# Kernel optimization log

Hardware: AMD Instinct MI355X
Metric: run time of the kernel (lower is better)

## Reference

```python
import jax, jax.numpy as jnp
import numpy as np

N_NODES = 100000
N_EDGES = 1600000
NUM_FEATURES = 256
HIDDEN_DIM = 128
NUM_CLASSES = 16


def setup_inputs() -> dict:
    key = jax.random.key(0)
    k1, k2, k3, k4 = jax.random.split(key, 4)
    x = jax.random.normal(k1, (N_NODES, NUM_FEATURES), dtype=jnp.float32)
    edge_index = jax.random.randint(k2, (2, N_EDGES), 0, N_NODES, dtype=jnp.int64)
    # Glorot-style init like PyG GCNConv's Linear
    W1 = jax.random.normal(k3, (NUM_FEATURES, HIDDEN_DIM), dtype=jnp.float32) / np.sqrt(NUM_FEATURES)
    b1 = jnp.zeros((HIDDEN_DIM,), dtype=jnp.float32)
    W2 = jax.random.normal(k4, (HIDDEN_DIM, NUM_CLASSES), dtype=jnp.float32) / np.sqrt(HIDDEN_DIM)
    b2 = jnp.zeros((NUM_CLASSES,), dtype=jnp.float32)
    return {"x": x, "edge_index": edge_index, "W1": W1, "b1": b1, "W2": W2, "b2": b2}


def _gcn_norm(edge_index, num_nodes):
    """PyG GCNConv default: add self-loops, symmetric deg^{-1/2} A deg^{-1/2} norm."""
    loops = jnp.arange(num_nodes, dtype=edge_index.dtype)
    row = jnp.concatenate([edge_index[0], loops])  # source
    col = jnp.concatenate([edge_index[1], loops])  # target
    deg = jax.ops.segment_sum(jnp.ones_like(col, dtype=jnp.float32), col,
                              num_segments=num_nodes)
    dinv = jnp.where(deg > 0, jax.lax.rsqrt(deg), 0.0)
    norm = dinv[row] * dinv[col]  # [E + N]
    return row, col, norm


def _gcn_conv(h, row, col, norm, num_nodes):
    # transform first (PyG: lin then propagate), then normalized sum-aggregate
    msg = h[row] * norm[:, None]            # [E+N, d] gather + scale
    return jax.ops.segment_sum(msg, col, num_segments=num_nodes)


def reference(x, edge_index, W1, b1, W2, b2):
    num_nodes = x.shape[0]
    row, col, norm = _gcn_norm(edge_index, num_nodes)
    h = x @ W1
    h = _gcn_conv(h, row, col, norm, num_nodes) + b1
    h = jax.nn.relu(h)
    h = h @ W2
    out = _gcn_conv(h, row, col, norm, num_nodes) + b2
    return out
```

## Files before the change

kernel.cpp:

```cpp
#include <hip/hip_runtime.h>

#define N_NODES 100000
#define N_EDGES 1600000
#define F_IN    256
#define F_HID   128
#define F_OUT   16

#define BSHIFT  9
#define BNODES  512
#define NB      196
#define ECAP    16384
#define CHUNK   4096
#define NCHUNK  ((N_EDGES + CHUNK - 1) / CHUNK)

typedef __attribute__((ext_vector_type(8))) short short8;
typedef __attribute__((ext_vector_type(4))) float float4v;

typedef __attribute__((address_space(1))) const void g_void;
typedef __attribute__((address_space(3))) void lds_void;

__device__ __forceinline__ unsigned int bf16_rn(float f) {
    unsigned int u = __float_as_uint(f);
    return (u + 0x7FFFu + ((u >> 16) & 1u)) >> 16;
}
__device__ __forceinline__ unsigned int cvtpk(float lo, float hi) {
    unsigned int r;
    asm("v_cvt_pk_bf16_f32 %0, %1, %2" : "=v"(r) : "v"(lo), "v"(hi));
    return r;
}
__device__ __forceinline__ float blo(unsigned int u) { return __uint_as_float(u << 16); }
__device__ __forceinline__ float bhi(unsigned int u) { return __uint_as_float(u & 0xFFFF0000u); }
__device__ __forceinline__ float bfu(unsigned short u) { return __uint_as_float(((unsigned int)u) << 16); }


__global__ __launch_bounds__(256) void k_binit(int* __restrict__ bcur) {
    int i = threadIdx.x;
    if (i < NB) bcur[i] = i * ECAP;
}

__global__ __launch_bounds__(256) void k_binscatter(const int* __restrict__ rowi,
                                                    const int* __restrict__ coli,
                                                    int* __restrict__ bcur,
                                                    unsigned int* __restrict__ ebuf) {
    __shared__ int cnt[NB], gbase[NB], run[NB];
    int tid = threadIdx.x;
    int e0 = blockIdx.x * CHUNK;
    for (int i = tid; i < NB; i += 256) { cnt[i] = 0; run[i] = 0; }
    __syncthreads();
    int d[16], s[16];
    #pragma unroll
    for (int i = 0; i < 16; i++) {
        int e = e0 + i * 256 + tid;
        if (e < N_EDGES) {
            d[i] = coli[e]; s[i] = rowi[e];
            atomicAdd(&cnt[d[i] >> BSHIFT], 1);
        } else d[i] = -1;
    }
    __syncthreads();
    for (int i = tid; i < NB; i += 256)
        gbase[i] = cnt[i] ? atomicAdd(&bcur[i], cnt[i]) : 0;
    __syncthreads();
    #pragma unroll
    for (int i = 0; i < 16; i++) {
        if (d[i] >= 0) {
            int b = d[i] >> BSHIFT;
            int off = atomicAdd(&run[b], 1);
            ebuf[gbase[b] + off] = ((unsigned int)(d[i] & 511) << 17) | (unsigned int)s[i];
        }
    }
}

__global__ __launch_bounds__(512) void k_finalize(const int* __restrict__ bcur,
                                                  const unsigned int* __restrict__ ebuf,
                                                  int* __restrict__ rp_start,
                                                  int* __restrict__ rp_end,
                                                  float* __restrict__ dinv,
                                                  int* __restrict__ esrc) {
    __shared__ int ndeg[BNODES];
    __shared__ int sc[BNODES];
    int tid = threadIdx.x;
    int b   = blockIdx.x;
    int nb0 = b << BSHIFT;
    int ebeg = b * ECAP, eend = bcur[b];
    ndeg[tid] = 0;
    __syncthreads();
    for (int e = ebeg + tid; e < eend; e += 512)
        atomicAdd(&ndeg[ebuf[e] >> 17], 1);
    __syncthreads();
    sc[tid] = ndeg[tid];
    __syncthreads();
    for (int off = 1; off < BNODES; off <<= 1) {
        int v = (tid >= off) ? sc[tid - off] : 0;
        __syncthreads();
        sc[tid] += v;
        __syncthreads();
    }
    {
        int n = nb0 + tid;
        int deg = ndeg[tid];
        int excl = sc[tid] - deg;
        if (n < N_NODES) {
            rp_start[n] = ebeg + excl;
            rp_end[n]   = ebeg + excl + deg;
            dinv[n]     = rsqrtf(1.0f + (float)deg);
        }
        ndeg[tid] = excl;
    }
    __syncthreads();
    for (int e = ebeg + tid; e < eend; e += 512) {
        unsigned int p = ebuf[e];
        int off = atomicAdd(&ndeg[p >> 17], 1);
        esrc[ebeg + off] = (int)(p & 0x1FFFFu);
    }
}


__global__ __launch_bounds__(256) void k_transW(const float* __restrict__ W1,
                                                ushort* __restrict__ Wt) {
    int t = blockIdx.x * 256 + threadIdx.x;
    int c = t & 127, k = t >> 7;
    Wt[c * 256 + k] = (ushort)cvtpk(W1[k * 128 + c], 0.f);
}


__global__ __launch_bounds__(256) void k_gemm1(const float* __restrict__ x,
                                               const ushort* __restrict__ Wt,
                                               const float* __restrict__ dinv,
                                               ushort* __restrict__ g1) {
    __shared__ float lx[2][128][32];
    const int tid = threadIdx.x;
    const int wv = tid >> 6;
    const int l  = tid & 63;
    const int m  = l & 15;
    const int q  = l >> 4;
    const int R0 = blockIdx.x * 128;

    #pragma unroll
    for (int r = 0; r < 4; r++) {
        int rt = r * 32 + wv * 8 + (l >> 3);
        int c16 = l & 7;
        int grow = R0 + rt; if (grow > N_NODES - 1) grow = N_NODES - 1;
        const float* src = x + (size_t)grow * F_IN + ((c16 ^ (rt & 7)) << 2);
        float* dst = &lx[0][r * 32 + wv * 8][0];
        __builtin_amdgcn_global_load_lds((g_void*)src, (lds_void*)dst, 16, 0, 0);
    }

    short8 wf[2][8];
    #pragma unroll
    for (int ng = 0; ng < 2; ng++)
        #pragma unroll
        for (int kt = 0; kt < 8; kt++)
            wf[ng][kt] = *(const short8*)&Wt[(wv * 32 + ng * 16 + m) * 256 + kt * 32 + q * 8];

    float4v acc[8][2];
    #pragma unroll
    for (int rg = 0; rg < 8; rg++) {
        acc[rg][0] = (float4v){0.f, 0.f, 0.f, 0.f};
        acc[rg][1] = (float4v){0.f, 0.f, 0.f, 0.f};
    }

    __syncthreads();

    #pragma unroll
    for (int kt = 0; kt < 8; kt++) {
        const int buf = kt & 1;
        if (kt < 7) {
            #pragma unroll
            for (int r = 0; r < 4; r++) {
                int rt = r * 32 + wv * 8 + (l >> 3);
                int c16 = l & 7;
                int grow = R0 + rt; if (grow > N_NODES - 1) grow = N_NODES - 1;
                const float* src = x + (size_t)grow * F_IN + (kt + 1) * 32
                                     + ((c16 ^ (rt & 7)) << 2);
                float* dst = &lx[buf ^ 1][r * 32 + wv * 8][0];
                __builtin_amdgcn_global_load_lds((g_void*)src, (lds_void*)dst, 16, 0, 0);
            }
        }
        #pragma unroll
        for (int rg = 0; rg < 8; rg++) {
            int rt = rg * 16 + m, sw = rt & 7;
            float4 e0 = *(const float4*)&lx[buf][rt][((2 * q)     ^ sw) * 4];
            float4 e1 = *(const float4*)&lx[buf][rt][((2 * q + 1) ^ sw) * 4];
            short8 af;
            ((uint*)&af)[0] = cvtpk(e0.x, e0.y); ((uint*)&af)[1] = cvtpk(e0.z, e0.w);
            ((uint*)&af)[2] = cvtpk(e1.x, e1.y); ((uint*)&af)[3] = cvtpk(e1.z, e1.w);
            acc[rg][0] = __builtin_amdgcn_mfma_f32_16x16x32_bf16(af, wf[0][kt], acc[rg][0], 0, 0, 0);
            acc[rg][1] = __builtin_amdgcn_mfma_f32_16x16x32_bf16(af, wf[1][kt], acc[rg][1], 0, 0, 0);
        }
        __syncthreads();
    }

    #pragma unroll
    for (int rg = 0; rg < 8; rg++) {
        #pragma unroll
        for (int r = 0; r < 4; r++) {
            int row = R0 + rg * 16 + q * 4 + r;
            if (row < N_NODES) {
                float dv = dinv[row];
                float f0 = dv * acc[rg][0][r];
                float f1 = dv * acc[rg][1][r];
                g1[row * F_HID + wv * 32 + m]      = (ushort)cvtpk(f0, f0);
                g1[row * F_HID + wv * 32 + 16 + m] = (ushort)cvtpk(f1, f1);
            }
        }
    }
}


__global__ __launch_bounds__(256) void k_agg1g2(const int* __restrict__ rp_start,
                                                const int* __restrict__ rp_end,
                                                const int* __restrict__ esrc,
                                                const float* __restrict__ dinv,
                                                const unsigned int* __restrict__ g1,
                                                const float* __restrict__ b1,
                                                const float* __restrict__ W2,
                                                ushort* __restrict__ g2b,
                                                int nbase) {
    __shared__ float hl[4][132];
    const int tid  = threadIdx.x;
    const int wave = tid >> 6;
    const int lane = tid & 63;
    const int col  = lane & 15, part = lane >> 4;

    float w2r[32];
    #pragma unroll
    for (int i = 0; i < 32; i++) w2r[i] = W2[i * 64 + lane];

    float2 bb = ((const float2*)b1)[lane];

    #pragma unroll 1
    for (int j = 0; j < 4; j++) {
        const int node = nbase + blockIdx.x * 16 + j * 4 + wave;
        int s = rp_start[node], t = rp_end[node];
        unsigned int u = g1[node * 64 + lane];
        float ax = blo(u), ay = bhi(u);
        int e = s;
        for (; e + 7 < t; e += 8) {
            int r0 = esrc[e],     r1 = esrc[e + 1], r2 = esrc[e + 2], r3 = esrc[e + 3];
            int r4 = esrc[e + 4], r5 = esrc[e + 5], r6 = esrc[e + 6], r7 = esrc[e + 7];
            unsigned int u0 = g1[r0 * 64 + lane], u1 = g1[r1 * 64 + lane];
            unsigned int u2 = g1[r2 * 64 + lane], u3 = g1[r3 * 64 + lane];
            unsigned int u4 = g1[r4 * 64 + lane], u5 = g1[r5 * 64 + lane];
            unsigned int u6 = g1[r6 * 64 + lane], u7 = g1[r7 * 64 + lane];
            ax += blo(u0) + blo(u1) + blo(u2) + blo(u3)
                + blo(u4) + blo(u5) + blo(u6) + blo(u7);
            ay += bhi(u0) + bhi(u1) + bhi(u2) + bhi(u3)
                + bhi(u4) + bhi(u5) + bhi(u6) + bhi(u7);
        }
        for (; e + 3 < t; e += 4) {
            int r0 = esrc[e], r1 = esrc[e + 1], r2 = esrc[e + 2], r3 = esrc[e + 3];
            unsigned int u0 = g1[r0 * 64 + lane], u1 = g1[r1 * 64 + lane];
            unsigned int u2 = g1[r2 * 64 + lane], u3 = g1[r3 * 64 + lane];
            ax += blo(u0) + blo(u1) + blo(u2) + blo(u3);
            ay += bhi(u0) + bhi(u1) + bhi(u2) + bhi(u3);
        }
        for (; e < t; e++) {
            unsigned int u0 = g1[esrc[e] * 64 + lane];
            ax += blo(u0); ay += bhi(u0);
        }
        float wv = dinv[node];
        hl[wave][lane * 2]     = fmaxf(fmaf(wv, ax, bb.x), 0.0f);
        hl[wave][lane * 2 + 1] = fmaxf(fmaf(wv, ay, bb.y), 0.0f);

        float acc = 0.f;
        #pragma unroll
        for (int i = 0; i < 32; i++)
            acc = fmaf(hl[wave][i * 4 + part], w2r[i], acc);
        acc += __shfl_xor(acc, 16);
        acc += __shfl_xor(acc, 32);
        if (lane < 16) g2b[node * 16 + col] = (ushort)bf16_rn(wv * acc);
    }
}


__global__ __launch_bounds__(256) void k_agg2(const int* __restrict__ rp_start,
                                              const int* __restrict__ rp_end,
                                              const int* __restrict__ esrc,
                                              const float* __restrict__ dinv,
                                              const ushort* __restrict__ g2b,
                                              const float* __restrict__ b2,
                                              float* __restrict__ out) {
    int gid = blockIdx.x * 256 + threadIdx.x;
    int node = gid >> 4;
    int f = gid & 15;
    if (node >= N_NODES) return;
    int s = rp_start[node], t = rp_end[node];
    float acc = bfu(g2b[node * 16 + f]);
    int e = s;
    for (; e + 7 < t; e += 8) {
        float a0 = bfu(g2b[esrc[e] * 16 + f]),     a1 = bfu(g2b[esrc[e + 1] * 16 + f]);
        float a2 = bfu(g2b[esrc[e + 2] * 16 + f]), a3 = bfu(g2b[esrc[e + 3] * 16 + f]);
        float a4 = bfu(g2b[esrc[e + 4] * 16 + f]), a5 = bfu(g2b[esrc[e + 5] * 16 + f]);
        float a6 = bfu(g2b[esrc[e + 6] * 16 + f]), a7 = bfu(g2b[esrc[e + 7] * 16 + f]);
        acc += a0 + a1 + a2 + a3 + a4 + a5 + a6 + a7;
    }
    for (; e + 3 < t; e += 4) {
        acc += bfu(g2b[esrc[e] * 16 + f]) + bfu(g2b[esrc[e + 1] * 16 + f])
             + bfu(g2b[esrc[e + 2] * 16 + f]) + bfu(g2b[esrc[e + 3] * 16 + f]);
    }
    for (; e < t; e++) acc += bfu(g2b[esrc[e] * 16 + f]);
    out[node * 16 + f] = fmaf(dinv[node], acc, b2[f]);
}


extern "C" void kernel_launch(void* const* d_in, const int* in_sizes, int n_in,
                              void* d_out, int out_size, void* d_ws, size_t ws_size,
                              hipStream_t stream) {
    const float* x   = (const float*)d_in[0];
    const int*   ei  = (const int*)d_in[1];
    const float* W1  = (const float*)d_in[2];
    const float* b1  = (const float*)d_in[3];
    const float* W2  = (const float*)d_in[4];
    const float* b2  = (const float*)d_in[5];
    float* out = (float*)d_out;

    const int* rowi = ei;
    const int* coli = ei + N_EDGES;

    char* ws = (char*)d_ws;
    int*          bcur     = (int*)(ws + 0);
    int*          rp_start = (int*)(ws + 8192);
    int*          rp_end   = (int*)(ws + 524288);
    float*        dinv     = (float*)(ws + 1048576);
    unsigned int* ebuf     = (unsigned int*)(ws + 2097152);
    int*          esrc     = (int*)(ws + 16777216);
    ushort*       Wt       = (ushort*)(ws + 31457280);
    ushort*       g1       = (ushort*)(ws + 33554432);
    ushort*       g2b      = (ushort*)(ws + 62914560);

    k_binit     <<<1, 256, 0, stream>>>(bcur);
    k_binscatter<<<NCHUNK, 256, 0, stream>>>(rowi, coli, bcur, ebuf);
    k_finalize  <<<NB, 512, 0, stream>>>(bcur, ebuf, rp_start, rp_end, dinv, esrc);
    k_transW    <<<128, 256, 0, stream>>>(W1, Wt);

    k_gemm1     <<<(N_NODES + 127) / 128, 256, 0, stream>>>(x, Wt, dinv, g1);
    k_agg1g2    <<<N_NODES / 32, 256, 0, stream>>>(rp_start, rp_end, esrc, dinv,
                                                   (const unsigned int*)g1, b1, W2, g2b, 0);
    k_agg1g2    <<<N_NODES / 32, 256, 0, stream>>>(rp_start, rp_end, esrc, dinv,
                                                   (const unsigned int*)g1, b1, W2, g2b,
                                                   N_NODES / 2);
    k_agg2      <<<(N_NODES * 16 + 255) / 256, 256, 0, stream>>>(rp_start, rp_end, esrc,
                                                                 dinv, g2b, b2, out);
}
```

Baseline: 328.6 us.

## Replace LDS staging in GEMM1 with register double-buffered loads; split aggregation launches

After: 356.3 us. +8.4%, slower.

```diff
diff --git a/kernel.cpp b/kernel.cpp
--- a/kernel.cpp
+++ b/kernel.cpp
@@ -15,9 +15,6 @@
 
 typedef __attribute__((ext_vector_type(8))) short short8;
 typedef __attribute__((ext_vector_type(4))) float float4v;
-
-typedef __attribute__((address_space(1))) const void g_void;
-typedef __attribute__((address_space(3))) void lds_void;
 
 __device__ __forceinline__ unsigned int bf16_rn(float f) {
     unsigned int u = __float_as_uint(f);
@@ -127,7 +124,6 @@
                                                const ushort* __restrict__ Wt,
                                                const float* __restrict__ dinv,
                                                ushort* __restrict__ g1) {
-    __shared__ float lx[2][128][32];
     const int tid = threadIdx.x;
     const int wv = tid >> 6;
     const int l  = tid & 63;
@@ -135,16 +131,6 @@
     const int q  = l >> 4;
     const int R0 = blockIdx.x * 128;
 
-    #pragma unroll
-    for (int r = 0; r < 4; r++) {
-        int rt = r * 32 + wv * 8 + (l >> 3);
-        int c16 = l & 7;
-        int grow = R0 + rt; if (grow > N_NODES - 1) grow = N_NODES - 1;
-        const float* src = x + (size_t)grow * F_IN + ((c16 ^ (rt & 7)) << 2);
-        float* dst = &lx[0][r * 32 + wv * 8][0];
-        __builtin_amdgcn_global_load_lds((g_void*)src, (lds_void*)dst, 16, 0, 0);
-    }
-
     short8 wf[2][8];
     #pragma unroll
     for (int ng = 0; ng < 2; ng++)
@@ -152,58 +138,56 @@
         for (int kt = 0; kt < 8; kt++)
             wf[ng][kt] = *(const short8*)&Wt[(wv * 32 + ng * 16 + m) * 256 + kt * 32 + q * 8];
 
-    float4v acc[8][2];
-    #pragma unroll
-    for (int rg = 0; rg < 8; rg++) {
-        acc[rg][0] = (float4v){0.f, 0.f, 0.f, 0.f};
-        acc[rg][1] = (float4v){0.f, 0.f, 0.f, 0.f};
-    }
-
-    __syncthreads();
-
-    #pragma unroll
-    for (int kt = 0; kt < 8; kt++) {
-        const int buf = kt & 1;
-        if (kt < 7) {
-            #pragma unroll
-            for (int r = 0; r < 4; r++) {
-                int rt = r * 32 + wv * 8 + (l >> 3);
-                int c16 = l & 7;
-                int grow = R0 + rt; if (grow > N_NODES - 1) grow = N_NODES - 1;
-                const float* src = x + (size_t)grow * F_IN + (kt + 1) * 32
-                                     + ((c16 ^ (rt & 7)) << 2);
-                float* dst = &lx[buf ^ 1][r * 32 + wv * 8][0];
-                __builtin_amdgcn_global_load_lds((g_void*)src, (lds_void*)dst, 16, 0, 0);
-            }
-        }
-        #pragma unroll
-        for (int rg = 0; rg < 8; rg++) {
-            int rt = rg * 16 + m, sw = rt & 7;
-            float4 e0 = *(const float4*)&lx[buf][rt][((2 * q)     ^ sw) * 4];
-            float4 e1 = *(const float4*)&lx[buf][rt][((2 * q + 1) ^ sw) * 4];
-            short8 af;
-            ((uint*)&af)[0] = cvtpk(e0.x, e0.y); ((uint*)&af)[1] = cvtpk(e0.z, e0.w);
-            ((uint*)&af)[2] = cvtpk(e1.x, e1.y); ((uint*)&af)[3] = cvtpk(e1.z, e1.w);
-            acc[rg][0] = __builtin_amdgcn_mfma_f32_16x16x32_bf16(af, wf[0][kt], acc[rg][0], 0, 0, 0);
-            acc[rg][1] = __builtin_amdgcn_mfma_f32_16x16x32_bf16(af, wf[1][kt], acc[rg][1], 0, 0, 0);
-        }
-        __syncthreads();
-    }
-
-    #pragma unroll
-    for (int rg = 0; rg < 8; rg++) {
-        #pragma unroll
-        for (int r = 0; r < 4; r++) {
-            int row = R0 + rg * 16 + q * 4 + r;
-            if (row < N_NODES) {
-                float dv = dinv[row];
-                float f0 = dv * acc[rg][0][r];
-                float f1 = dv * acc[rg][1][r];
-                g1[row * F_HID + wv * 32 + m]      = (ushort)cvtpk(f0, f0);
-                g1[row * F_HID + wv * 32 + 16 + m] = (ushort)cvtpk(f1, f1);
-            }
-        }
-    }
+#define ROWPTR(rg) ({ int grow_ = R0 + (rg) * 16 + m;                          \
+                      if (grow_ > N_NODES - 1) grow_ = N_NODES - 1;            \
+                      x + (size_t)grow_ * F_IN + q * 8; })
+
+#define LOADRG(buf, rg) { const float* p_ = ROWPTR(rg);                        \
+    _Pragma("unroll")                                                          \
+    for (int kt_ = 0; kt_ < 8; kt_++) {                                        \
+        buf[2 * kt_]     = *(const float4*)&p_[kt_ * 32];                      \
+        buf[2 * kt_ + 1] = *(const float4*)&p_[kt_ * 32 + 4];                  \
+    } }
+
+#define CONSUME(buf, rg) {                                                     \
+    float4v a0_ = (float4v){0.f, 0.f, 0.f, 0.f};                               \
+    float4v a1_ = (float4v){0.f, 0.f, 0.f, 0.f};                               \
+    _Pragma("unroll")                                                          \
+    for (int kt_ = 0; kt_ < 8; kt_++) {                                        \
+        short8 af_;                                                            \
+        ((uint*)&af_)[0] = cvtpk(buf[2 * kt_].x,     buf[2 * kt_].y);          \
+        ((uint*)&af_)[1] = cvtpk(buf[2 * kt_].z,     buf[2 * kt_].w);          \
+        ((uint*)&af_)[2] = cvtpk(buf[2 * kt_ + 1].x, buf[2 * kt_ + 1].y);      \
+        ((uint*)&af_)[3] = cvtpk(buf[2 * kt_ + 1].z, buf[2 * kt_ + 1].w);      \
+        a0_ = __builtin_amdgcn_mfma_f32_16x16x32_bf16(af_, wf[0][kt_], a0_, 0, 0, 0); \
+        a1_ = __builtin_amdgcn_mfma_f32_16x16x32_bf16(af_, wf[1][kt_], a1_, 0, 0, 0); \
+    }                                                                          \
+    _Pragma("unroll")                                                          \
+    for (int r_ = 0; r_ < 4; r_++) {                                           \
+        int row_ = R0 + (rg) * 16 + q * 4 + r_;                                \
+        if (row_ < N_NODES) {                                                  \
+            float dv_ = dinv[row_];                                            \
+            float f0_ = dv_ * a0_[r_];                                         \
+            float f1_ = dv_ * a1_[r_];                                         \
+            g1[row_ * F_HID + wv * 32 + m]      = (ushort)cvtpk(f0_, f0_);     \
+            g1[row_ * F_HID + wv * 32 + 16 + m] = (ushort)cvtpk(f1_, f1_);     \
+        }                                                                      \
+    } }
+
+    float4 xa[16], xb[16];
+    LOADRG(xa, 0);
+    LOADRG(xb, 1);
+    CONSUME(xa, 0);  LOADRG(xa, 2);
+    CONSUME(xb, 1);  LOADRG(xb, 3);
+    CONSUME(xa, 2);  LOADRG(xa, 4);
+    CONSUME(xb, 3);  LOADRG(xb, 5);
+    CONSUME(xa, 4);  LOADRG(xa, 6);
+    CONSUME(xb, 5);  LOADRG(xb, 7);
+    CONSUME(xa, 6);
+    CONSUME(xb, 7);
+#undef ROWPTR
+#undef LOADRG
+#undef CONSUME
 }
 
 
@@ -215,7 +199,7 @@
                                                 const float* __restrict__ b1,
                                                 const float* __restrict__ W2,
                                                 ushort* __restrict__ g2b,
-                                                int nbase) {
+                                                int nbase, int nend) {
     __shared__ float hl[4][132];
     const int tid  = threadIdx.x;
     const int wave = tid >> 6;
@@ -231,6 +215,7 @@
     #pragma unroll 1
     for (int j = 0; j < 4; j++) {
         const int node = nbase + blockIdx.x * 16 + j * 4 + wave;
+        if (node >= nend) continue;
         int s = rp_start[node], t = rp_end[node];
         unsigned int u = g1[node * 64 + lane];
         float ax = blo(u), ay = bhi(u);
@@ -334,11 +319,12 @@
     k_transW    <<<128, 256, 0, stream>>>(W1, Wt);
 
     k_gemm1     <<<(N_NODES + 127) / 128, 256, 0, stream>>>(x, Wt, dinv, g1);
-    k_agg1g2    <<<N_NODES / 32, 256, 0, stream>>>(rp_start, rp_end, esrc, dinv,
-                                                   (const unsigned int*)g1, b1, W2, g2b, 0);
-    k_agg1g2    <<<N_NODES / 32, 256, 0, stream>>>(rp_start, rp_end, esrc, dinv,
-                                                   (const unsigned int*)g1, b1, W2, g2b,
-                                                   N_NODES / 2);
+    for (int qd = 0; qd < 4; qd++) {
+        int nbase = qd * 25000;
+        k_agg1g2 <<<(25000 + 15) / 16, 256, 0, stream>>>(rp_start, rp_end, esrc, dinv,
+                                                         (const unsigned int*)g1, b1, W2,
+                                                         g2b, nbase, nbase + 25000);
+    }
     k_agg2      <<<(N_NODES * 16 + 255) / 256, 256, 0, stream>>>(rp_start, rp_end, esrc,
                                                                  dinv, g2b, b2, out);
 }
```
